# Performance work log

Hardware: AMD Instinct MI355X
Metric: run time of the kernel (lower is better)

## Reference

```python
import jax, jax.numpy as jnp
import numpy as np


def _qkernel(r, i, j, k):
    # Build the real-valued block kernel of a quaternion dense layer.
    # r,i,j,k: [in/4, out/4] -> kernel [in, out] implementing the Hamilton product.
    col_r = jnp.concatenate([r, -i, -j, -k], axis=0)
    col_i = jnp.concatenate([i, r, -k, j], axis=0)
    col_j = jnp.concatenate([j, k, r, -i], axis=0)
    col_k = jnp.concatenate([k, -j, i, r], axis=0)
    return jnp.concatenate([col_r, col_i, col_j, col_k], axis=1)


def setup_inputs() -> dict:
    key = jax.random.key(0)
    ks = jax.random.split(key, 12)
    B, F, H = 32768, 1024, 256
    F4, H4 = F // 4, H // 4
    s_in = 1.0 / np.sqrt(F)
    s_h = 1.0 / np.sqrt(H)
    inp = {
        "x": jax.random.normal(ks[0], (B, F), dtype=jnp.float32),
        "wx_r": jax.random.normal(ks[1], (4, F4, H4), dtype=jnp.float32) * s_in,
        "wx_i": jax.random.normal(ks[2], (4, F4, H4), dtype=jnp.float32) * s_in,
        "wx_j": jax.random.normal(ks[3], (4, F4, H4), dtype=jnp.float32) * s_in,
        "wx_k": jax.random.normal(ks[4], (4, F4, H4), dtype=jnp.float32) * s_in,
        "bx": jnp.zeros((4, H), dtype=jnp.float32),
        "uh_r": jax.random.normal(ks[5], (4, H4, H4), dtype=jnp.float32) * s_h,
        "uh_i": jax.random.normal(ks[6], (4, H4, H4), dtype=jnp.float32) * s_h,
        "uh_j": jax.random.normal(ks[7], (4, H4, H4), dtype=jnp.float32) * s_h,
        "uh_k": jax.random.normal(ks[8], (4, H4, H4), dtype=jnp.float32) * s_h,
        "fco_w": jax.random.normal(ks[9], (H, H), dtype=jnp.float32) * s_h,
        "fco_b": jnp.zeros((H,), dtype=jnp.float32),
    }
    return inp


def reference(x, wx_r, wx_i, wx_j, wx_k, bx, uh_r, uh_i, uh_j, uh_k, fco_w, fco_b):
    # Single-step quaternion LSTM cell with zero initial hidden/cell state.
    # Gate order along leading axis: [forget, input, output, cell].
    Kx = jax.vmap(_qkernel)(wx_r, wx_i, wx_j, wx_k)   # [4, F, H]
    Ku = jax.vmap(_qkernel)(uh_r, uh_i, uh_j, uh_k)   # [4, H, H]
    H = bx.shape[1]
    h0 = jnp.zeros((x.shape[0], H), dtype=x.dtype)
    c0 = h0
    gx = jnp.einsum('bf,gfh->gbh', x, Kx) + bx[:, None, :]   # [4, B, H]
    gu = jnp.einsum('bh,ghk->gbk', h0, Ku)                    # [4, B, H]
    z = gx + gu
    ft = jax.nn.sigmoid(z[0])
    it = jax.nn.sigmoid(z[1])
    ot = jax.nn.sigmoid(z[2])
    at = z[3]
    c = it * jnp.tanh(at) + ft * c0
    h = ot * jnp.tanh(c)
    return h @ fco_w + fco_b
```

## Files before the change

### kernel.cpp

```cpp
#include <hip/hip_runtime.h>
#include <cstdint>
#include <cstddef>

#define WS_WP   0
#define WS_FCO  1572864
#define WS_BP   1703936
#define WS_HVP  1707008

typedef __attribute__((ext_vector_type(8))) __bf16 bf16x8;
typedef __attribute__((ext_vector_type(4))) float floatx4;

__device__ __forceinline__ unsigned short f2bf(float f) {
  unsigned int u = __builtin_bit_cast(unsigned int, f);
  u += 0x7fffu + ((u >> 16) & 1u);
  return (unsigned short)(u >> 16);
}

__device__ __forceinline__ float sigmf(float z) {
  return __builtin_amdgcn_rcpf(1.f + __expf(-z));
}
__device__ __forceinline__ float tanh_(float z) {
  return 1.f - 2.f * __builtin_amdgcn_rcpf(1.f + __expf(2.f * z));
}

__device__ __forceinline__ void gld16(const void* g, void* l) {
  __builtin_amdgcn_global_load_lds(
      (const __attribute__((address_space(1))) unsigned int*)g,
      (__attribute__((address_space(3))) unsigned int*)l, 16, 0, 0);
}

__global__ __launch_bounds__(256) void pack_w_k(
    const float* __restrict__ wr, const float* __restrict__ wi,
    const float* __restrict__ wj, const float* __restrict__ wk,
    const float* __restrict__ bx, unsigned short* __restrict__ Wp,
    float* __restrict__ bp) {
  int id = blockIdx.x * 256 + threadIdx.x;
  int c = id >> 7, oct = id & 127;
  int gp = c % 3 + 1;
  int h = c / 3;
  int hb = h >> 6, hr = h & 63;
  int f0 = oct << 3;
  int fb = f0 >> 8, fr0 = f0 & 255;
  const int   comp_t[4][4] = {{0,1,2,3},{1,0,3,2},{2,3,0,1},{3,2,1,0}};
  const float sign_t[4][4] = {{1.f,-1.f,-1.f,-1.f},{1.f,1.f,-1.f,1.f},
                              {1.f,1.f,1.f,-1.f},{1.f,-1.f,1.f,1.f}};
  const float* srcs[4] = {wr, wi, wj, wk};
  const float* s = srcs[comp_t[hb][fb]] + ((size_t)((gp << 8) + fr0)) * 64 + hr;
  float sg = sign_t[hb][fb];
  unsigned short v[8];
#pragma unroll
  for (int j = 0; j < 8; ++j) v[j] = f2bf(sg * s[(size_t)j * 64]);
  int cb = c / 96, nl = c % 96;
  int kb = f0 >> 5, q = (f0 >> 3) & 3;
  int idx16 = (nl << 2) + (q ^ ((nl >> 1) & 3));
  unsigned short* dst = Wp + (size_t)((cb << 5) + kb) * 3072 + idx16 * 8;
  uint4 val = make_uint4(
      (unsigned)v[0] | ((unsigned)v[1] << 16), (unsigned)v[2] | ((unsigned)v[3] << 16),
      (unsigned)v[4] | ((unsigned)v[5] << 16), (unsigned)v[6] | ((unsigned)v[7] << 16));
  *(uint4*)dst = val;
  if (oct == 0) bp[c] = bx[(gp << 8) + h];
}

__global__ __launch_bounds__(256) void pack_fco_k(
    const float* __restrict__ fw, unsigned short* __restrict__ Fp) {
  int id = blockIdx.x * 256 + threadIdx.x;
  int n = id >> 5, oct = id & 31;
  int k0 = oct << 3;
  unsigned short v[8];
#pragma unroll
  for (int j = 0; j < 8; ++j) v[j] = f2bf(fw[(size_t)(k0 + j) * 256 + n]);
  int nb = n >> 7, nl = n & 127, kb = oct >> 2, q = oct & 3;
  int idx16 = (nl << 2) + (q ^ ((nl >> 1) & 3));
  unsigned short* dst = Fp + (size_t)((nb << 3) + kb) * 4096 + idx16 * 8;
  uint4 val = make_uint4(
      (unsigned)v[0] | ((unsigned)v[1] << 16), (unsigned)v[2] | ((unsigned)v[3] << 16),
      (unsigned)v[4] | ((unsigned)v[5] << 16), (unsigned)v[6] | ((unsigned)v[7] << 16));
  *(uint4*)dst = val;
}

__global__ __launch_bounds__(256, 4) void gemm1_k(
    const float* __restrict__ x, const unsigned short* __restrict__ Wp,
    const float* __restrict__ bp, unsigned short* __restrict__ hvp) {
  __shared__ char smem[25600];
  unsigned short* sA = (unsigned short*)smem;
  unsigned short* sB = (unsigned short*)(smem + 10240);
  float* zep = (float*)smem;

  const int t = threadIdx.x;
  const int lane = t & 63, wid = t >> 6;
  const int wm = wid >> 1, wn = wid & 1;
  const int lrow = lane & 15, q = lane >> 4;
  const int row0 = blockIdx.x * 128;
  const int cb = blockIdx.y;
  const float* xbase = x + (size_t)row0 * 1024;

  floatx4 acc[4][3];
#pragma unroll
  for (int i = 0; i < 4; ++i)
#pragma unroll
    for (int j = 0; j < 3; ++j) acc[i][j] = (floatx4){0.f, 0.f, 0.f, 0.f};

  for (int kt = 0; kt < 32; ++kt) {
    const int k0 = kt * 32;
    const unsigned short* bt = Wp + (size_t)((cb << 5) + kt) * 3072;
    gld16(bt + t * 8, sB + t * 8);
    if (t < 128) gld16(bt + 2048 + t * 8, sB + 2048 + t * 8);
#pragma unroll
    for (int i = 0; i < 4; ++i) {
      int task = t + i * 256;
      int r = task >> 3, f4 = task & 7;
      float4 d = *(const float4*)(xbase + (size_t)r * 1024 + k0 + f4 * 4);
      unsigned int p0 = (unsigned)f2bf(d.x) | ((unsigned)f2bf(d.y) << 16);
      unsigned int p1 = (unsigned)f2bf(d.z) | ((unsigned)f2bf(d.w) << 16);
      *(uint2*)(sA + r * 40 + f4 * 4) = make_uint2(p0, p1);
    }
    __syncthreads();
    bf16x8 af[4], bf[3];
#pragma unroll
    for (int mt = 0; mt < 4; ++mt)
      af[mt] = *(const bf16x8*)(const void*)(sA + (wm * 64 + mt * 16 + lrow) * 40 + q * 8);
#pragma unroll
    for (int nt = 0; nt < 3; ++nt) {
      int n = wn * 48 + nt * 16 + lrow;
      int off16 = (n << 2) + (q ^ ((n >> 1) & 3));
      bf[nt] = *(const bf16x8*)(const void*)(sB + off16 * 8);
    }
#pragma unroll
    for (int mt = 0; mt < 4; ++mt)
#pragma unroll
      for (int nt = 0; nt < 3; ++nt)
        acc[mt][nt] = __builtin_amdgcn_mfma_f32_16x16x32_bf16(af[mt], bf[nt], acc[mt][nt], 0, 0, 0);
    __syncthreads();
  }

  const float* bp0 = bp + cb * 96;
  const int erow = t >> 2, eoct = t & 3;
#pragma unroll
  for (int pass = 0; pass < 2; ++pass) {
    if (wm == pass) {
#pragma unroll
      for (int mt = 0; mt < 4; ++mt)
#pragma unroll
        for (int nt = 0; nt < 3; ++nt)
#pragma unroll
          for (int r = 0; r < 4; ++r)
            zep[(mt * 16 + q * 4 + r) * 100 + wn * 48 + nt * 16 + lrow] = acc[mt][nt][r];
    }
    __syncthreads();
    unsigned short v[8];
#pragma unroll
    for (int j = 0; j < 8; ++j) {
      int hp = eoct * 8 + j;
      float zi = zep[erow * 100 + hp * 3 + 0] + bp0[hp * 3 + 0];
      float zo = zep[erow * 100 + hp * 3 + 1] + bp0[hp * 3 + 1];
      float zc = zep[erow * 100 + hp * 3 + 2] + bp0[hp * 3 + 2];
      float it = sigmf(zi);
      float ot = sigmf(zo);
      float cc = it * tanh_(zc);
      v[j] = f2bf(ot * tanh_(cc));
    }
    int ml = pass * 64 + erow;
    int idx16 = (ml << 2) + (eoct ^ ((ml >> 1) & 3));
    uint4 val = make_uint4(
        (unsigned)v[0] | ((unsigned)v[1] << 16), (unsigned)v[2] | ((unsigned)v[3] << 16),
        (unsigned)v[4] | ((unsigned)v[5] << 16), (unsigned)v[6] | ((unsigned)v[7] << 16));
    *(uint4*)(hvp + (size_t)(blockIdx.x * 8 + cb) * 4096 + idx16 * 8) = val;
    __syncthreads();
  }
}

__global__ __launch_bounds__(256, 3) void gemm2_k(
    const unsigned short* __restrict__ hvp, const unsigned short* __restrict__ Fp,
    const float* __restrict__ fcob, float* __restrict__ out) {
  __shared__ char smem[16384];
  unsigned short* sA = (unsigned short*)smem;
  unsigned short* sB = (unsigned short*)(smem + 8192);
  const int t = threadIdx.x;
  const int lane = t & 63, wid = t >> 6;
  const int wm = wid >> 1, wn = wid & 1;
  const int lrow = lane & 15, q = lane >> 4;
  const int mb = blockIdx.x, nb = blockIdx.y;

  floatx4 acc[4][4];
#pragma unroll
  for (int i = 0; i < 4; ++i)
#pragma unroll
    for (int j = 0; j < 4; ++j) acc[i][j] = (floatx4){0.f, 0.f, 0.f, 0.f};

  for (int kt = 0; kt < 8; ++kt) {
    const unsigned short* at_ = hvp + (size_t)(mb * 8 + kt) * 4096;
    const unsigned short* bt_ = Fp + (size_t)(nb * 8 + kt) * 4096;
    gld16(at_ + t * 8, sA + t * 8);
    gld16(at_ + 2048 + t * 8, sA + 2048 + t * 8);
    gld16(bt_ + t * 8, sB + t * 8);
    gld16(bt_ + 2048 + t * 8, sB + 2048 + t * 8);
    __syncthreads();
    bf16x8 af[4], bf[4];
#pragma unroll
    for (int mt = 0; mt < 4; ++mt) {
      int m = wm * 64 + mt * 16 + lrow;
      int o = (m << 2) + (q ^ ((m >> 1) & 3));
      af[mt] = *(const bf16x8*)(const void*)(sA + o * 8);
    }
#pragma unroll
    for (int nt = 0; nt < 4; ++nt) {
      int n = wn * 64 + nt * 16 + lrow;
      int o = (n << 2) + (q ^ ((n >> 1) & 3));
      bf[nt] = *(const bf16x8*)(const void*)(sB + o * 8);
    }
#pragma unroll
    for (int mt = 0; mt < 4; ++mt)
#pragma unroll
      for (int nt = 0; nt < 4; ++nt)
        acc[mt][nt] = __builtin_amdgcn_mfma_f32_16x16x32_bf16(af[mt], bf[nt], acc[mt][nt], 0, 0, 0);
    __syncthreads();
  }
#pragma unroll
  for (int nt = 0; nt < 4; ++nt) {
    int colg = nb * 128 + wn * 64 + nt * 16 + lrow;
    float bias = fcob[colg];
#pragma unroll
    for (int mt = 0; mt < 4; ++mt) {
      int rowg = mb * 128 + wm * 64 + mt * 16 + q * 4;
#pragma unroll
      for (int r = 0; r < 4; ++r)
        out[(size_t)(rowg + r) * 256 + colg] = acc[mt][nt][r] + bias;
    }
  }
}

extern "C" void kernel_launch(void* const* d_in, const int* in_sizes, int n_in,
                              void* d_out, int out_size, void* d_ws, size_t ws_size,
                              hipStream_t stream) {
  const float* x  = (const float*)d_in[0];
  const float* wr = (const float*)d_in[1];
  const float* wi = (const float*)d_in[2];
  const float* wj = (const float*)d_in[3];
  const float* wk = (const float*)d_in[4];
  const float* bx = (const float*)d_in[5];
  const float* fw = (const float*)d_in[10];
  const float* fb = (const float*)d_in[11];
  char* ws = (char*)d_ws;
  unsigned short* Wp  = (unsigned short*)(ws + WS_WP);
  unsigned short* Fp  = (unsigned short*)(ws + WS_FCO);
  float*          bp  = (float*)(ws + WS_BP);
  unsigned short* hvp = (unsigned short*)(ws + WS_HVP);
  float*          out = (float*)d_out;

  hipLaunchKernelGGL(pack_w_k,   dim3(384),    dim3(256), 0, stream, wr, wi, wj, wk, bx, Wp, bp);
  hipLaunchKernelGGL(pack_fco_k, dim3(32),     dim3(256), 0, stream, fw, Fp);
  hipLaunchKernelGGL(gemm1_k,    dim3(256, 8), dim3(256), 0, stream, x, Wp, bp, hvp);
  hipLaunchKernelGGL(gemm2_k,    dim3(256, 2), dim3(256), 0, stream, hvp, Fp, fb, out);
}
```

Measured before the change: 313.5 us.

## Double gemm1 N-tile and load fp32 x directly into LDS via async copies

Each gemm1 block now covers 192 gate columns instead of 96, so the grid shrinks from 8 to 4 column blocks and every x tile is read from HBM half as often. The x tile is copied as fp32 into swizzled LDS with async global-to-LDS loads, replacing the register load and bf16 convert before the store. Conversion to bf16 now happens when fragments are read from LDS. LDS use and accumulator registers double, and occupancy drops from 4 to 2 blocks per CU, which reduces latency hiding.

Measured after the change: 295.8 us. -5.7%, faster.

```diff
diff --git a/kernel.cpp b/kernel.cpp
--- a/kernel.cpp
+++ b/kernel.cpp
@@ -50,10 +50,10 @@
   unsigned short v[8];
 #pragma unroll
   for (int j = 0; j < 8; ++j) v[j] = f2bf(sg * s[(size_t)j * 64]);
-  int cb = c / 96, nl = c % 96;
+  int cb = c / 192, nl = c % 192;
   int kb = f0 >> 5, q = (f0 >> 3) & 3;
   int idx16 = (nl << 2) + (q ^ ((nl >> 1) & 3));
-  unsigned short* dst = Wp + (size_t)((cb << 5) + kb) * 3072 + idx16 * 8;
+  unsigned short* dst = Wp + (size_t)(cb * 32 + kb) * 6144 + idx16 * 8;
   uint4 val = make_uint4(
       (unsigned)v[0] | ((unsigned)v[1] << 16), (unsigned)v[2] | ((unsigned)v[3] << 16),
       (unsigned)v[4] | ((unsigned)v[5] << 16), (unsigned)v[6] | ((unsigned)v[7] << 16));
@@ -78,12 +78,12 @@
   *(uint4*)dst = val;
 }
 
-__global__ __launch_bounds__(256, 4) void gemm1_k(
+__global__ __launch_bounds__(256, 2) void gemm1_k(
     const float* __restrict__ x, const unsigned short* __restrict__ Wp,
     const float* __restrict__ bp, unsigned short* __restrict__ hvp) {
-  __shared__ char smem[25600];
-  unsigned short* sA = (unsigned short*)smem;
-  unsigned short* sB = (unsigned short*)(smem + 10240);
+  __shared__ char smem[51456];
+  float* sAf = (float*)smem;
+  unsigned short* sBs = (unsigned short*)(smem + 16384);
   float* zep = (float*)smem;
 
   const int t = threadIdx.x;
@@ -91,80 +91,92 @@
   const int wm = wid >> 1, wn = wid & 1;
   const int lrow = lane & 15, q = lane >> 4;
   const int row0 = blockIdx.x * 128;
-  const int cb = blockIdx.y;
+  const int cby = blockIdx.y;
   const float* xbase = x + (size_t)row0 * 1024;
 
-  floatx4 acc[4][3];
+  floatx4 acc[4][6];
 #pragma unroll
   for (int i = 0; i < 4; ++i)
 #pragma unroll
-    for (int j = 0; j < 3; ++j) acc[i][j] = (floatx4){0.f, 0.f, 0.f, 0.f};
+    for (int j = 0; j < 6; ++j) acc[i][j] = (floatx4){0.f, 0.f, 0.f, 0.f};
 
   for (int kt = 0; kt < 32; ++kt) {
     const int k0 = kt * 32;
-    const unsigned short* bt = Wp + (size_t)((cb << 5) + kt) * 3072;
-    gld16(bt + t * 8, sB + t * 8);
-    if (t < 128) gld16(bt + 2048 + t * 8, sB + 2048 + t * 8);
 #pragma unroll
     for (int i = 0; i < 4; ++i) {
-      int task = t + i * 256;
-      int r = task >> 3, f4 = task & 7;
-      float4 d = *(const float4*)(xbase + (size_t)r * 1024 + k0 + f4 * 4);
-      unsigned int p0 = (unsigned)f2bf(d.x) | ((unsigned)f2bf(d.y) << 16);
-      unsigned int p1 = (unsigned)f2bf(d.z) | ((unsigned)f2bf(d.w) << 16);
-      *(uint2*)(sA + r * 40 + f4 * 4) = make_uint2(p0, p1);
-    }
-    __syncthreads();
-    bf16x8 af[4], bf[3];
+      int s = t + i * 256;
+      int m = s >> 3, j = s & 7, jj = j ^ (m & 7);
+      gld16(xbase + (size_t)m * 1024 + k0 + jj * 4, sAf + s * 4);
+    }
+    const unsigned short* bt = Wp + (size_t)(cby * 32 + kt) * 6144;
+#pragma unroll
+    for (int i = 0; i < 3; ++i) {
+      int s = t + i * 256;
+      gld16(bt + s * 8, sBs + s * 8);
+    }
+    __syncthreads();
+    bf16x8 af[4], bf[6];
+#pragma unroll
+    for (int mt = 0; mt < 4; ++mt) {
+      int m = wm * 64 + mt * 16 + lrow;
+      const float4 a0 = *(const float4*)(sAf + (m * 8 + ((2 * q) ^ (m & 7))) * 4);
+      const float4 a1 = *(const float4*)(sAf + (m * 8 + ((2 * q + 1) ^ (m & 7))) * 4);
+      bf16x8 v;
+      v[0] = (__bf16)a0.x; v[1] = (__bf16)a0.y; v[2] = (__bf16)a0.z; v[3] = (__bf16)a0.w;
+      v[4] = (__bf16)a1.x; v[5] = (__bf16)a1.y; v[6] = (__bf16)a1.z; v[7] = (__bf16)a1.w;
+      af[mt] = v;
+    }
+#pragma unroll
+    for (int nt = 0; nt < 6; ++nt) {
+      int n = wn * 96 + nt * 16 + lrow;
+      int off16 = (n << 2) + (q ^ ((n >> 1) & 3));
+      bf[nt] = *(const bf16x8*)(const void*)(sBs + off16 * 8);
+    }
 #pragma unroll
     for (int mt = 0; mt < 4; ++mt)
-      af[mt] = *(const bf16x8*)(const void*)(sA + (wm * 64 + mt * 16 + lrow) * 40 + q * 8);
-#pragma unroll
-    for (int nt = 0; nt < 3; ++nt) {
-      int n = wn * 48 + nt * 16 + lrow;
-      int off16 = (n << 2) + (q ^ ((n >> 1) & 3));
-      bf[nt] = *(const bf16x8*)(const void*)(sB + off16 * 8);
-    }
-#pragma unroll
-    for (int mt = 0; mt < 4; ++mt)
-#pragma unroll
-      for (int nt = 0; nt < 3; ++nt)
+#pragma unroll
+      for (int nt = 0; nt < 6; ++nt)
         acc[mt][nt] = __builtin_amdgcn_mfma_f32_16x16x32_bf16(af[mt], bf[nt], acc[mt][nt], 0, 0, 0);
     __syncthreads();
   }
 
-  const float* bp0 = bp + cb * 96;
-  const int erow = t >> 2, eoct = t & 3;
+  const float* bp0 = bp + cby * 192;
+  const int er = t >> 2, oc = t & 3;
 #pragma unroll
   for (int pass = 0; pass < 2; ++pass) {
     if (wm == pass) {
 #pragma unroll
       for (int mt = 0; mt < 4; ++mt)
 #pragma unroll
-        for (int nt = 0; nt < 3; ++nt)
+        for (int nt = 0; nt < 6; ++nt)
 #pragma unroll
           for (int r = 0; r < 4; ++r)
-            zep[(mt * 16 + q * 4 + r) * 100 + wn * 48 + nt * 16 + lrow] = acc[mt][nt][r];
-    }
-    __syncthreads();
-    unsigned short v[8];
-#pragma unroll
-    for (int j = 0; j < 8; ++j) {
-      int hp = eoct * 8 + j;
-      float zi = zep[erow * 100 + hp * 3 + 0] + bp0[hp * 3 + 0];
-      float zo = zep[erow * 100 + hp * 3 + 1] + bp0[hp * 3 + 1];
-      float zc = zep[erow * 100 + hp * 3 + 2] + bp0[hp * 3 + 2];
-      float it = sigmf(zi);
-      float ot = sigmf(zo);
-      float cc = it * tanh_(zc);
-      v[j] = f2bf(ot * tanh_(cc));
-    }
-    int ml = pass * 64 + erow;
-    int idx16 = (ml << 2) + (eoct ^ ((ml >> 1) & 3));
-    uint4 val = make_uint4(
-        (unsigned)v[0] | ((unsigned)v[1] << 16), (unsigned)v[2] | ((unsigned)v[3] << 16),
-        (unsigned)v[4] | ((unsigned)v[5] << 16), (unsigned)v[6] | ((unsigned)v[7] << 16));
-    *(uint4*)(hvp + (size_t)(blockIdx.x * 8 + cb) * 4096 + idx16 * 8) = val;
+            zep[(mt * 16 + q * 4 + r) * 201 + wn * 96 + nt * 16 + lrow] = acc[mt][nt][r];
+    }
+    __syncthreads();
+    int ml = pass * 64 + er;
+#pragma unroll
+    for (int half = 0; half < 2; ++half) {
+      int oo = oc + half * 4;
+      unsigned short v[8];
+#pragma unroll
+      for (int j = 0; j < 8; ++j) {
+        int hl = oo * 8 + j;
+        float zi = zep[er * 201 + hl * 3 + 0] + bp0[hl * 3 + 0];
+        float zo = zep[er * 201 + hl * 3 + 1] + bp0[hl * 3 + 1];
+        float zc = zep[er * 201 + hl * 3 + 2] + bp0[hl * 3 + 2];
+        float it = sigmf(zi);
+        float ot = sigmf(zo);
+        float cc = it * tanh_(zc);
+        v[j] = f2bf(ot * tanh_(cc));
+      }
+      int ktile = cby * 2 + (oo >> 2), qq = oo & 3;
+      int idx16 = (ml << 2) + (qq ^ ((ml >> 1) & 3));
+      uint4 val = make_uint4(
+          (unsigned)v[0] | ((unsigned)v[1] << 16), (unsigned)v[2] | ((unsigned)v[3] << 16),
+          (unsigned)v[4] | ((unsigned)v[5] << 16), (unsigned)v[6] | ((unsigned)v[7] << 16));
+      *(uint4*)(hvp + (size_t)(blockIdx.x * 8 + ktile) * 4096 + idx16 * 8) = val;
+    }
     __syncthreads();
   }
 }
@@ -249,6 +261,6 @@
 
   hipLaunchKernelGGL(pack_w_k,   dim3(384),    dim3(256), 0, stream, wr, wi, wj, wk, bx, Wp, bp);
   hipLaunchKernelGGL(pack_fco_k, dim3(32),     dim3(256), 0, stream, fw, Fp);
-  hipLaunchKernelGGL(gemm1_k,    dim3(256, 8), dim3(256), 0, stream, x, Wp, bp, hvp);
+  hipLaunchKernelGGL(gemm1_k,    dim3(256, 4), dim3(256), 0, stream, x, Wp, bp, hvp);
   hipLaunchKernelGGL(gemm2_k,    dim3(256, 2), dim3(256), 0, stream, hvp, Fp, fb, out);
 }
```
